# Kernel tuning notes

Measured on AMD Instinct MI355X. Metric: run time of the kernel, lower is better.

Reference implementation:

```python
import jax, jax.numpy as jnp
import numpy as np
import math

S, B, H, NH = 2048, 2, 2048, 16
HD = H // NH
COEFF = 1.0  # layer_number = 1
NORM = math.sqrt(HD) * COEFF
MASK_VAL = -10000.0


def setup_inputs() -> dict:
    key = jax.random.key(0)
    ks = jax.random.split(key, 4)
    hidden_states = jax.random.normal(ks[0], (S, B, H), dtype=jnp.float32)
    # causal mask: True = masked (Megatron convention)
    attention_mask = jnp.triu(jnp.ones((S, S), dtype=bool), k=1)[None, None]
    w_qkv = jax.random.normal(ks[1], (H, 3 * H), dtype=jnp.float32) * (1.0 / math.sqrt(H))
    b_qkv = jnp.zeros((3 * H,), dtype=jnp.float32)
    w_dense = jax.random.normal(ks[2], (H, H), dtype=jnp.float32) * (1.0 / math.sqrt(H))
    b_dense = jnp.zeros((H,), dtype=jnp.float32)
    return {"hidden_states": hidden_states, "attention_mask": attention_mask,
            "w_qkv": w_qkv, "b_qkv": b_qkv, "w_dense": w_dense, "b_dense": b_dense}


def reference(hidden_states, attention_mask, w_qkv, b_qkv, w_dense, b_dense):
    s, b, h = hidden_states.shape
    # QKV projection: [s, b, 3h] -> [s, b, nh, 3*hd] -> split
    mixed = hidden_states @ w_qkv + b_qkv
    mixed = mixed.reshape(s, b, NH, 3 * HD)
    q, k, v = jnp.split(mixed, 3, axis=-1)  # each [s, b, nh, hd]
    # raw scores scaled by 1/(sqrt(hd)*coeff)  -> [b, nh, s_q, s_k]
    scores = jnp.einsum('sbnd,tbnd->bnst', q, k) / NORM
    # fused scale-mask-softmax in fp32 with scale=coeff (net 1/sqrt(hd))
    scores32 = scores.astype(jnp.float32) * COEFF
    scores32 = jnp.where(attention_mask, MASK_VAL, scores32)
    probs = jax.nn.softmax(scores32, axis=-1).astype(hidden_states.dtype)
    # dropout p=0.0 -> identity
    context = jnp.einsum('bnst,tbnd->sbnd', probs, v).reshape(s, b, h)
    # row-parallel dense with skip_bias_add: bias returned separately
    output = context @ w_dense
    return output, b_dense
```

## Files before the change

### kernel.cpp

```cpp
#include <hip/hip_runtime.h>
#include <hip/hip_bf16.h>

constexpr int S   = 2048;
constexpr int B   = 2;
constexpr int H   = 2048;
constexpr int NH  = 16;
constexpr int HD  = 128;
constexpr int K3H = 3 * H;
constexpr float SCALE2 = 0.08838834764831845f * 1.4426950408889634f;
constexpr float MSHIFT = 12.0f;

typedef __attribute__((ext_vector_type(8))) short short8;
typedef __attribute__((ext_vector_type(4))) float f32x4;

__device__ __forceinline__ ushort f2b(float f) {
  uint u = __float_as_uint(f);
  return (ushort)((u + 0x7fffu + ((u >> 16) & 1u)) >> 16);
}

__device__ __forceinline__ f32x4 mfma16(short8 a, short8 b, f32x4 c) {
  return __builtin_amdgcn_mfma_f32_16x16x32_bf16(a, b, c, 0, 0, 0);
}

__device__ __forceinline__ void gld16(const ushort* g, ushort* l) {
  __builtin_amdgcn_global_load_lds((const __attribute__((address_space(1))) void*)g,
                                   (__attribute__((address_space(3))) void*)l,
                                   16, 0, 0);
}

__global__ __launch_bounds__(256) void cast_bf16(const float* __restrict__ src,
                                                 ushort* __restrict__ dst, int n) {
  int i = (blockIdx.x * 256 + threadIdx.x) * 4;
  if (i >= n) return;
  float4 v = *(const float4*)(src + i);
  ushort4 o;
  o.x = f2b(v.x); o.y = f2b(v.y); o.z = f2b(v.z); o.w = f2b(v.w);
  *(ushort4*)(dst + i) = o;
}

__global__ __launch_bounds__(256) void transpose_cast(const float* __restrict__ src,
                                                      ushort* __restrict__ dst,
                                                      int R, int C) {
  __shared__ ushort tile[32][33];
  int c0 = blockIdx.x * 32, r0 = blockIdx.y * 32;
  int tx = threadIdx.x, ty = threadIdx.y;
#pragma unroll
  for (int i = 0; i < 4; i++) {
    int r = r0 + ty + i * 8;
    tile[ty + i * 8][tx] = f2b(src[(size_t)r * C + c0 + tx]);
  }
  __syncthreads();
#pragma unroll
  for (int i = 0; i < 4; i++) {
    int c = c0 + ty + i * 8;
    dst[(size_t)c * R + r0 + tx] = tile[tx][ty + i * 8];
  }
}

template <int MODE>
__global__ __launch_bounds__(256) void gemm_bt(const ushort* __restrict__ A,
                                               const ushort* __restrict__ Bt,
                                               const float* __restrict__ bias,
                                               void* __restrict__ out0,
                                               void* __restrict__ out1,
                                               int M, int N, int K) {
  __shared__ ushort lds_a[128 * 64];
  __shared__ ushort lds_b[128 * 64];
  const int tid  = threadIdx.x;
  const int wave = tid >> 6, lane = tid & 63;
  const int quad = lane >> 4, l15 = lane & 15;
  const int wr = wave >> 1, wc = wave & 1;
  const int m0 = blockIdx.y * 128, n0 = blockIdx.x * 128;

  f32x4 acc[4][4] = {};

  const int srow   = tid >> 3;
  const int schunk = (tid & 7) ^ (srow & 7);
  const ushort* gaS = A  + (size_t)(m0 + srow) * K + schunk * 8;
  const ushort* gbS = Bt + (size_t)(n0 + srow) * K + schunk * 8;

  const int fsw = l15 & 7;

  const int nk = K >> 6;
  for (int kt = 0; kt < nk; kt++) {
    const int ko = kt * 64;
#pragma unroll
    for (int j = 0; j < 4; j++) {
      gld16(gaS + (size_t)(j * 32) * K + ko, &lds_a[(j * 256 + wave * 64) * 8]);
      gld16(gbS + (size_t)(j * 32) * K + ko, &lds_b[(j * 256 + wave * 64) * 8]);
    }
    __syncthreads();

#pragma unroll
    for (int ks = 0; ks < 2; ks++) {
      short8 af[4], bq[4];
#pragma unroll
      for (int mt = 0; mt < 4; mt++)
        af[mt] = *(const short8*)&lds_a[((wr * 64 + mt * 16 + l15) * 8 + ((ks * 4 + quad) ^ fsw)) * 8];
#pragma unroll
      for (int nt = 0; nt < 4; nt++)
        bq[nt] = *(const short8*)&lds_b[((wc * 64 + nt * 16 + l15) * 8 + ((ks * 4 + quad) ^ fsw)) * 8];
#pragma unroll
      for (int mt = 0; mt < 4; mt++)
#pragma unroll
        for (int nt = 0; nt < 4; nt++)
          acc[mt][nt] = mfma16(af[mt], bq[nt], acc[mt][nt]);
    }
    __syncthreads();
  }

  if (MODE == 1) {
#pragma unroll
    for (int nt = 0; nt < 4; nt++) {
      const int col = n0 + wc * 64 + nt * 16 + l15;
      const int nh  = col / 384;
      const int rem = col - nh * 384;
      const float bv = bias[col];
      if (rem < 256) {
        ushort* qk = (ushort*)out0;
#pragma unroll
        for (int mt = 0; mt < 4; mt++) {
          const int rb = m0 + wr * 64 + mt * 16 + quad * 4;
#pragma unroll
          for (int i = 0; i < 4; i++)
            qk[((size_t)(rb + i) * NH + nh) * 256 + rem] = f2b(acc[mt][nt][i] + bv);
        }
      } else {
        ushort* vt = (ushort*)out1;
        const size_t colbase = ((size_t)nh * 128 + (rem - 256)) * S;
#pragma unroll
        for (int mt = 0; mt < 4; mt++) {
          const int rb = m0 + wr * 64 + mt * 16 + quad * 4;
#pragma unroll
          for (int i = 0; i < 4; i++) {
            const int row = rb + i;
            vt[(size_t)(row & 1) * ((size_t)NH * 128 * S) + colbase + (row >> 1)]
                = f2b(acc[mt][nt][i] + bv);
          }
        }
      }
    }
  } else {
    float* Co = (float*)out0;
#pragma unroll
    for (int mt = 0; mt < 4; mt++)
#pragma unroll
      for (int nt = 0; nt < 4; nt++) {
        const int col = n0 + wc * 64 + nt * 16 + l15;
#pragma unroll
        for (int i = 0; i < 4; i++) {
          const int row = m0 + wr * 64 + mt * 16 + quad * 4 + i;
          Co[(size_t)row * N + col] = acc[mt][nt][i];
        }
      }
  }
}

__global__ __launch_bounds__(512) void flash_attn(const ushort* __restrict__ qkb,
                                                  const ushort* __restrict__ VtG,
                                                  ushort* __restrict__ ctxb) {
  __shared__ ushort Ks[2][64 * 128];
  __shared__ ushort Vt[2][128 * 64];
  __shared__ ushort Pls[8][16 * 64];

  const int tid  = threadIdx.x;
  const int wave = tid >> 6, lane = tid & 63;
  const int quad = lane >> 4, l15 = lane & 15;
  const int jj = blockIdx.x;
  const int nh = blockIdx.y, b = blockIdx.z;
  const int stA = jj, stB = 15 - jj;
  const int nA = 2 * jj + 2;
  constexpr int TOT = 34;

  ushort* Pw = Pls[wave];

  const int ktRow = tid >> 4;
  const int kCol  = (tid & 15) ^ (ktRow & 15);
  const ushort* kS = qkb + (((size_t)(ktRow * B + b) * NH + nh) * 256 + 128 + kCol * 8);
  const int vdRow = tid >> 3;
  const int vCol  = (tid & 7) ^ (vdRow & 7);
  const ushort* vS = VtG + ((size_t)(b * NH + nh) * 128 + vdRow) * (size_t)S + vCol * 8;

  const size_t kRowStep32 = (size_t)32 * B * NH * 256;
  const size_t vRowStep64 = (size_t)64 * S;
  const size_t kTileStep  = (size_t)64 * B * NH * 256;

  auto stageTile = [&](int kt, int nxt) {
    const size_t ko = (size_t)kt * kTileStep;
    const int vo = kt * 64;
    gld16(kS + ko, &Ks[nxt][(wave * 64) * 8]);
    gld16(kS + ko + kRowStep32, &Ks[nxt][(512 + wave * 64) * 8]);
    gld16(vS + vo, &Vt[nxt][(wave * 64) * 8]);
    gld16(vS + vo + vRowStep64, &Vt[nxt][(512 + wave * 64) * 8]);
  };

  short8 qf[4];
  int q0 = stA * 128;
  {
    const ushort* qPtr = qkb + (((size_t)((q0 + wave * 16 + l15) * B + b) * NH + nh) * 256 + quad * 8);
#pragma unroll
    for (int ks = 0; ks < 4; ks++) qf[ks] = *(const short8*)(qPtr + ks * 32);
  }

  float l_r[4];
  f32x4 acc_o[8];
#pragma unroll
  for (int i = 0; i < 4; i++) l_r[i] = 0.0f;
#pragma unroll
  for (int j = 0; j < 8; j++) acc_o[j] = (f32x4){0.f, 0.f, 0.f, 0.f};

  stageTile(0, 0);
  __syncthreads();

  for (int it = 0; it < TOT; it++) {
    const int buf = it & 1;
    const int kt = (it < nA) ? it : it - nA;
    const int t0 = kt * 64;

    if (it + 1 < TOT)
      stageTile((it + 1 < nA) ? it + 1 : it + 1 - nA, buf ^ 1);

    f32x4 sa[4];
#pragma unroll
    for (int nt = 0; nt < 4; nt++) sa[nt] = (f32x4){0.f, 0.f, 0.f, 0.f};
#pragma unroll
    for (int ks = 0; ks < 4; ks++) {
#pragma unroll
      for (int nt = 0; nt < 4; nt++) {
        const int gs = (ks * 4 + quad) ^ l15;
        short8 bq = *(const short8*)&Ks[buf][((nt * 16 + l15) * 16 + gs) * 8];
        sa[nt] = mfma16(qf[ks], bq, sa[nt]);
      }
    }

    const int qw0 = q0 + wave * 16;
    const bool diag = (t0 + 63 > qw0);
#pragma unroll
    for (int i = 0; i < 4; i++) {
      const int qg = qw0 + quad * 4 + i;
      const int prow = quad * 4 + i;
      float lacc = l_r[i];
#pragma unroll
      for (int nt = 0; nt < 4; nt++) {
        float e = fmaf(sa[nt][i], SCALE2, -MSHIFT);
        if (diag) {
          const int tg = t0 + nt * 16 + l15;
          if (tg > qg) e = -1e30f;
        }
        const float p = exp2f(e);
        lacc += p;
        const int gs = (nt * 2 + (l15 >> 3)) ^ (prow & 7);
        Pw[prow * 64 + gs * 8 + (l15 & 7)] = f2b(p);
      }
      l_r[i] = lacc;
    }

#pragma unroll
    for (int ks2 = 0; ks2 < 2; ks2++) {
      const int pg = (ks2 * 4 + quad) ^ (l15 & 7);
      short8 a2 = *(const short8*)&Pw[l15 * 64 + pg * 8];
#pragma unroll
      for (int j = 0; j < 8; j++) {
        const int gs = (ks2 * 4 + quad) ^ (l15 & 7);
        short8 b2 = *(const short8*)&Vt[buf][((j * 16 + l15) * 8 + gs) * 8];
        acc_o[j] = mfma16(a2, b2, acc_o[j]);
      }
    }

    if (it == nA - 1) {
#pragma unroll
      for (int i = 0; i < 4; i++) {
        float ls = l_r[i];
#pragma unroll
        for (int off = 1; off < 16; off <<= 1) ls += __shfl_xor(ls, off);
        const float inv = 1.0f / ls;
        const int qg = q0 + wave * 16 + quad * 4 + i;
        ushort* dst = ctxb + ((size_t)qg * B + b) * H + nh * HD;
#pragma unroll
        for (int j = 0; j < 8; j++)
          dst[j * 16 + l15] = f2b(acc_o[j][i] * inv);
      }
      q0 = stB * 128;
      const ushort* qPtr = qkb + (((size_t)((q0 + wave * 16 + l15) * B + b) * NH + nh) * 256 + quad * 8);
#pragma unroll
      for (int ks = 0; ks < 4; ks++) qf[ks] = *(const short8*)(qPtr + ks * 32);
#pragma unroll
      for (int i = 0; i < 4; i++) l_r[i] = 0.0f;
#pragma unroll
      for (int j = 0; j < 8; j++) acc_o[j] = (f32x4){0.f, 0.f, 0.f, 0.f};
    }

    __syncthreads();
  }

#pragma unroll
  for (int i = 0; i < 4; i++) {
    float ls = l_r[i];
#pragma unroll
    for (int off = 1; off < 16; off <<= 1) ls += __shfl_xor(ls, off);
    const float inv = 1.0f / ls;
    const int qg = q0 + wave * 16 + quad * 4 + i;
    ushort* dst = ctxb + ((size_t)qg * B + b) * H + nh * HD;
#pragma unroll
    for (int j = 0; j < 8; j++)
      dst[j * 16 + l15] = f2b(acc_o[j][i] * inv);
  }
}

extern "C" void kernel_launch(void* const* d_in, const int* in_sizes, int n_in,
                              void* d_out, int out_size, void* d_ws, size_t ws_size,
                              hipStream_t stream) {
  (void)in_sizes; (void)n_in; (void)out_size; (void)ws_size;
  const float* hs     = (const float*)d_in[0];
  const float* wqkv   = (const float*)d_in[2];
  const float* bqkv   = (const float*)d_in[3];
  const float* wdense = (const float*)d_in[4];
  const float* bdense = (const float*)d_in[5];
  float* out = (float*)d_out;

  ushort* Xb      = (ushort*)d_ws;
  ushort* WqkvT   = Xb      + (size_t)S * B * H;
  ushort* WdenseT = WqkvT   + (size_t)H * K3H;
  ushort* qkb     = WdenseT + (size_t)H * H;
  ushort* VtG     = qkb     + (size_t)S * B * NH * 256;
  ushort* ctxb    = VtG     + (size_t)B * NH * HD * S;

  cast_bf16<<<dim3((S * B * H) / 1024), dim3(256), 0, stream>>>(hs, Xb, S * B * H);
  transpose_cast<<<dim3(K3H / 32, H / 32), dim3(32, 8), 0, stream>>>(wqkv, WqkvT, H, K3H);
  transpose_cast<<<dim3(H / 32, H / 32), dim3(32, 8), 0, stream>>>(wdense, WdenseT, H, H);

  gemm_bt<1><<<dim3(K3H / 128, (S * B) / 128), dim3(256), 0, stream>>>(
      Xb, WqkvT, bqkv, qkb, VtG, S * B, K3H, H);

  flash_attn<<<dim3(8, NH, B), dim3(512), 0, stream>>>(qkb, VtG, ctxb);

  gemm_bt<0><<<dim3(H / 128, (S * B) / 128), dim3(256), 0, stream>>>(
      ctxb, WdenseT, nullptr, out, nullptr, S * B, H, H);

  hipMemcpyAsync(out + (size_t)S * B * H, bdense, H * sizeof(float),
                 hipMemcpyDeviceToDevice, stream);
}
```

Baseline: 404.0 us.

## Double-buffer GEMM LDS tiles with K-step of 32 to overlap loads

Reworks the bf16 GEMM main loop from a single 64-wide K tile to two 32-wide LDS buffers. The next tile is prefetched while MFMAs run on the current one, with only one barrier per iteration. The XOR swizzle is adapted to the new 32-element row layout. The aim is to hide global-to-LDS latency. The cost is twice as many loop iterations and barriers with half the MFMA work between them.

```diff
diff --git a/kernel.cpp b/kernel.cpp
--- a/kernel.cpp
+++ b/kernel.cpp
@@ -64,8 +64,8 @@
                                                void* __restrict__ out0,
                                                void* __restrict__ out1,
                                                int M, int N, int K) {
-  __shared__ ushort lds_a[128 * 64];
-  __shared__ ushort lds_b[128 * 64];
+  __shared__ ushort lds_a[2][128 * 32];
+  __shared__ ushort lds_b[2][128 * 32];
   const int tid  = threadIdx.x;
   const int wave = tid >> 6, lane = tid & 63;
   const int quad = lane >> 4, l15 = lane & 15;
@@ -74,38 +74,43 @@
 
   f32x4 acc[4][4] = {};
 
-  const int srow   = tid >> 3;
-  const int schunk = (tid & 7) ^ (srow & 7);
-  const ushort* gaS = A  + (size_t)(m0 + srow) * K + schunk * 8;
-  const ushort* gbS = Bt + (size_t)(n0 + srow) * K + schunk * 8;
-
-  const int fsw = l15 & 7;
-
-  const int nk = K >> 6;
+  const int srow = tid >> 2;
+  const int scol = ((tid & 3) ^ ((tid >> 3) & 3)) * 8;
+  const ushort* gaS = A  + (size_t)(m0 + srow) * K + scol;
+  const ushort* gbS = Bt + (size_t)(n0 + srow) * K + scol;
+  const size_t rowStep64 = (size_t)64 * K;
+
+  auto stage = [&](int kt, int nxt) {
+    const int ko = kt * 32;
+    gld16(gaS + ko, &lds_a[nxt][(wave * 64) * 8]);
+    gld16(gaS + rowStep64 + ko, &lds_a[nxt][(256 + wave * 64) * 8]);
+    gld16(gbS + ko, &lds_b[nxt][(wave * 64) * 8]);
+    gld16(gbS + rowStep64 + ko, &lds_b[nxt][(256 + wave * 64) * 8]);
+  };
+
+  const int fsw = (l15 >> 1) & 3;
+
+  const int nk = K >> 5;
+  stage(0, 0);
+  __syncthreads();
+
   for (int kt = 0; kt < nk; kt++) {
-    const int ko = kt * 64;
-#pragma unroll
-    for (int j = 0; j < 4; j++) {
-      gld16(gaS + (size_t)(j * 32) * K + ko, &lds_a[(j * 256 + wave * 64) * 8]);
-      gld16(gbS + (size_t)(j * 32) * K + ko, &lds_b[(j * 256 + wave * 64) * 8]);
-    }
-    __syncthreads();
-
-#pragma unroll
-    for (int ks = 0; ks < 2; ks++) {
-      short8 af[4], bq[4];
-#pragma unroll
-      for (int mt = 0; mt < 4; mt++)
-        af[mt] = *(const short8*)&lds_a[((wr * 64 + mt * 16 + l15) * 8 + ((ks * 4 + quad) ^ fsw)) * 8];
+    const int buf = kt & 1;
+    if (kt + 1 < nk) stage(kt + 1, buf ^ 1);
+
+    short8 af[4], bq[4];
+#pragma unroll
+    for (int mt = 0; mt < 4; mt++)
+      af[mt] = *(const short8*)&lds_a[buf][(wr * 64 + mt * 16 + l15) * 32 + ((quad ^ fsw)) * 8];
+#pragma unroll
+    for (int nt = 0; nt < 4; nt++)
+      bq[nt] = *(const short8*)&lds_b[buf][(wc * 64 + nt * 16 + l15) * 32 + ((quad ^ fsw)) * 8];
+#pragma unroll
+    for (int mt = 0; mt < 4; mt++)
 #pragma unroll
       for (int nt = 0; nt < 4; nt++)
-        bq[nt] = *(const short8*)&lds_b[((wc * 64 + nt * 16 + l15) * 8 + ((ks * 4 + quad) ^ fsw)) * 8];
-#pragma unroll
-      for (int mt = 0; mt < 4; mt++)
-#pragma unroll
-        for (int nt = 0; nt < 4; nt++)
-          acc[mt][nt] = mfma16(af[mt], bq[nt], acc[mt][nt]);
-    }
+        acc[mt][nt] = mfma16(af[mt], bq[nt], acc[mt][nt]);
+
     __syncthreads();
   }
 
```

Measured after the change: 410.1 us. No clear change (+1.5%).
